# Performance work log

Measured on AMD Instinct MI355X. Metric: run time of the kernel, lower is better.

Reference implementation:

```python
import jax, jax.numpy as jnp
import numpy as np

N_EMBED = 1024
N_HEAD = 16
EPS = 1.1920929e-07  # torch.finfo(float32).eps, nn.RMSNorm default eps=None


def rmsnorm(x, w):
    var = jnp.mean(x * x, axis=-1, keepdims=True)
    return x * jax.lax.rsqrt(var + EPS) * w


def setup_inputs() -> dict:
    key = jax.random.key(0)
    ks = jax.random.split(key, 12)
    d = N_EMBED
    s = lambda fan_in: 1.0 / np.sqrt(fan_in)
    inp = {
        "x": jax.random.normal(ks[0], (2, 2048, d), jnp.float32),
        "w_attn": jax.random.uniform(ks[1], (d, 3 * d), jnp.float32, -s(d), s(d)),
        "b_attn": jax.random.uniform(ks[2], (3 * d,), jnp.float32, -s(d), s(d)),
        "w_proj": jax.random.uniform(ks[3], (d, d), jnp.float32, -s(d), s(d)),
        "b_proj": jax.random.uniform(ks[4], (d,), jnp.float32, -s(d), s(d)),
        "w_fc1": jax.random.uniform(ks[5], (d, 4 * d), jnp.float32, -s(d), s(d)),
        "b_fc1": jax.random.uniform(ks[6], (4 * d,), jnp.float32, -s(d), s(d)),
        "w_fc2": jax.random.uniform(ks[7], (4 * d, d), jnp.float32, -s(4 * d), s(4 * d)),
        "b_fc2": jax.random.uniform(ks[8], (d,), jnp.float32, -s(4 * d), s(4 * d)),
        "g_norm1": jnp.ones((d,), jnp.float32),
        "g_norm2": jnp.ones((d,), jnp.float32),
    }
    return inp


def reference(x, w_attn, b_attn, w_proj, b_proj, w_fc1, b_fc1, w_fc2, b_fc2, g_norm1, g_norm2):
    B, T, d = x.shape
    H = N_HEAD
    hd = d // H

    # --- attention branch ---
    h = rmsnorm(x, g_norm1)
    qkv = h @ w_attn + b_attn  # [B,T,3d]
    q, k, v = jnp.split(qkv, 3, axis=-1)
    q = q.reshape(B, T, H, hd).transpose(0, 2, 1, 3)  # [B,H,T,hd]
    k = k.reshape(B, T, H, hd).transpose(0, 2, 1, 3)
    v = v.reshape(B, T, H, hd).transpose(0, 2, 1, 3)
    qk = jnp.einsum('bhqd,bhkd->bhqk', q, k)  # NOTE: no logit scaling (as in source)
    mask = jnp.tril(jnp.ones((T, T), bool))
    qk = jnp.where(mask, qk, -jnp.inf)
    # source scales softmax OUTPUT by n_embed**-0.5 (faithful quirk)
    attn = jax.nn.softmax(qk, axis=-1) * (d ** -0.5)
    o = jnp.einsum('bhqk,bhkd->bhqd', attn, v)
    o = o.transpose(0, 2, 1, 3).reshape(B, T, d)
    x = x + (o @ w_proj + b_proj)

    # --- MLP branch ---
    h = rmsnorm(x, g_norm2)
    h = jax.nn.gelu(h @ w_fc1 + b_fc1, approximate=False)
    x = x + (h @ w_fc2 + b_fc2)
    return x
```

## Files before the change

kernel.cpp:

```cpp
#include <hip/hip_runtime.h>
#include <hip/hip_bf16.h>


typedef __hip_bfloat16 bf16;
typedef __attribute__((ext_vector_type(8))) short short8;
typedef __attribute__((ext_vector_type(4))) float floatx4;

__device__ __forceinline__ float bits2f(unsigned short u) {
  union { unsigned int i; float f; } c; c.i = ((unsigned int)u) << 16; return c.f;
}
__device__ __forceinline__ unsigned short f2bits(float f) {
  bf16 b = __float2bfloat16(f);
  union { bf16 b; unsigned short u; } c; c.b = b; return c.u;
}

__device__ __forceinline__ void gld_lds16(const unsigned short* g, unsigned short* l) {
  __builtin_amdgcn_global_load_lds(
      (const __attribute__((address_space(1))) void*)g,
      (__attribute__((address_space(3))) void*)l, 16, 0, 0);
}

__global__ __launch_bounds__(256) void rmsnorm_r9(const float* __restrict__ x,
                                                  const float* __restrict__ g,
                                                  unsigned short* __restrict__ out)
{
  const int row = blockIdx.x, tid = threadIdx.x;
  const size_t rb = (size_t)row * 1024;
  float4 xv = *(const float4*)(x + rb + tid * 4);
  float v[4] = {xv.x, xv.y, xv.z, xv.w};
  float s = v[0]*v[0] + v[1]*v[1] + v[2]*v[2] + v[3]*v[3];
  #pragma unroll
  for (int off = 32; off > 0; off >>= 1) s += __shfl_down(s, off, 64);
  __shared__ float part[4];
  if ((tid & 63) == 0) part[tid >> 6] = s;
  __syncthreads();
  const float tot = part[0] + part[1] + part[2] + part[3];
  const float sc = rsqrtf(tot * (1.0f / 1024.0f) + 1.1920929e-07f);
  float4 gv = *(const float4*)(g + tid * 4);
  ushort4 o4 = { f2bits(v[0] * sc * gv.x), f2bits(v[1] * sc * gv.y),
                 f2bits(v[2] * sc * gv.z), f2bits(v[3] * sc * gv.w) };
  *(ushort4*)(out + rb + tid * 4) = o4;
}

__global__ __launch_bounds__(256) void wprep_r9(const float* __restrict__ in,
                                                unsigned short* __restrict__ out,
                                                int K, int N)
{
  __shared__ unsigned short tile[32][33];
  const int tid = threadIdx.x;
  const int k0 = blockIdx.y * 32, n0 = blockIdx.x * 32;
  const int tr = tid >> 3, tc4 = (tid & 7) * 4;
  float4 v = *(const float4*)(in + (size_t)(k0 + tr) * N + n0 + tc4);
  tile[tr][tc4 + 0] = f2bits(v.x);
  tile[tr][tc4 + 1] = f2bits(v.y);
  tile[tr][tc4 + 2] = f2bits(v.z);
  tile[tr][tc4 + 3] = f2bits(v.w);
  __syncthreads();
  ushort4 o = { tile[tc4 + 0][tr], tile[tc4 + 1][tr],
                tile[tc4 + 2][tr], tile[tc4 + 3][tr] };
  *(ushort4*)(out + (size_t)(n0 + tr) * K + k0 + tc4) = o;
}

template<int EPI>
__global__ __launch_bounds__(256) void gemm_r9(
    const unsigned short* __restrict__ A,
    const unsigned short* __restrict__ BT,
    const float* __restrict__ bias,
    const float* __restrict__ resid,
    void* __restrict__ Cout,
    int M, int N, int K)
{
  __shared__ __align__(16) unsigned short As[128 * 32];
  __shared__ __align__(16) unsigned short Bs[128 * 32];
  const int tid = threadIdx.x;
  const int lane = tid & 63;
  const int wv = tid >> 6;
  const int m0 = blockIdx.y * 128, n0 = blockIdx.x * 128;
  const int wm = (wv >> 1) * 64, wn = (wv & 1) * 64;

  const int s0 = tid, s1 = tid + 256;
  const int r0 = s0 >> 2, kq0 = (s0 & 3) ^ ((r0 >> 1) & 3);
  const int r1 = s1 >> 2, kq1 = (s1 & 3) ^ ((r1 >> 1) & 3);
  const unsigned short* Ab = A  + (size_t)m0 * K;
  const unsigned short* Bb = BT + (size_t)n0 * K;
  const size_t ga0 = (size_t)r0 * K + kq0 * 8;
  const size_t ga1 = (size_t)r1 * K + kq1 * 8;

  floatx4 acc[4][4];
  #pragma unroll
  for (int i = 0; i < 4; ++i)
    #pragma unroll
    for (int j = 0; j < 4; ++j)
      acc[i][j] = (floatx4){0.f, 0.f, 0.f, 0.f};

  int aoff[4], boff[4];
  #pragma unroll
  for (int i = 0; i < 4; ++i) {
    int ra = wm + i * 16 + (lane & 15);
    aoff[i] = (ra * 4 + ((lane >> 4) ^ ((ra >> 1) & 3))) * 8;
    int rb = wn + i * 16 + (lane & 15);
    boff[i] = (rb * 4 + ((lane >> 4) ^ ((rb >> 1) & 3))) * 8;
  }

  for (int k0 = 0; k0 < K; k0 += 32) {
    __syncthreads();
    gld_lds16(Ab + ga0 + k0, As + s0 * 8);
    gld_lds16(Ab + ga1 + k0, As + s1 * 8);
    gld_lds16(Bb + ga0 + k0, Bs + s0 * 8);
    gld_lds16(Bb + ga1 + k0, Bs + s1 * 8);
    __syncthreads();

    short8 af[4], bfr[4];
    #pragma unroll
    for (int i = 0; i < 4; ++i) {
      af[i]  = *(const short8*)(As + aoff[i]);
      bfr[i] = *(const short8*)(Bs + boff[i]);
    }
    #pragma unroll
    for (int i = 0; i < 4; ++i)
      #pragma unroll
      for (int j = 0; j < 4; ++j)
        acc[i][j] = __builtin_amdgcn_mfma_f32_16x16x32_bf16(af[i], bfr[j], acc[i][j], 0, 0, 0);
  }

  #pragma unroll
  for (int i = 0; i < 4; ++i) {
    #pragma unroll
    for (int j = 0; j < 4; ++j) {
      const int rbase = m0 + wm + i * 16 + (lane >> 4) * 4;
      const int c = n0 + wn + j * 16 + (lane & 15);
      const float bia = bias[c];
      #pragma unroll
      for (int r = 0; r < 4; ++r) {
        float v = acc[i][j][r] + bia;
        const size_t idx = (size_t)(rbase + r) * N + c;
        if constexpr (EPI == 0) {
          ((unsigned short*)Cout)[idx] = f2bits(v);
        } else if constexpr (EPI == 1) {
          ((float*)Cout)[idx] = v + resid[idx];
        } else if constexpr (EPI == 2) {
          v = 0.5f * v * (1.0f + erff(v * 0.70710678118654752f));
          ((unsigned short*)Cout)[idx] = f2bits(v);
        } else {
          ((float*)Cout)[idx] = v + resid[idx];
        }
      }
    }
  }
}

__global__ __launch_bounds__(512) void attn_r9(const unsigned short* __restrict__ qkv,
                                               unsigned short* __restrict__ o)
{
  __shared__ __align__(16) unsigned short Qs[128 * 64];
  __shared__ __align__(16) unsigned short Ks[2][64 * 64];
  __shared__ __align__(16) unsigned short VT[2][64 * 72];
  __shared__ __align__(16) unsigned short Ps[128 * 72];
  __shared__ __align__(16) float stat_s[128];

  const int tid = threadIdx.x, lane = tid & 63, wv = tid >> 6;
  const int quad = lane >> 4, l15 = lane & 15;
  const int qt0 = blockIdx.x, bh = blockIdx.y;
  const int b = bh >> 4, h = bh & 15;
  const size_t base = (size_t)b * 2048 * 3072;
  const int qcol = h * 64, kcol = 1024 + h * 64, vcol = 2048 + h * 64;

  const int sr = tid >> 3, scp = tid & 7, sc = scp ^ (sr & 7);
  const unsigned short* kgp = qkv + base + (size_t)sr * 3072 + kcol + sc * 8;
  const int vp = tid & 31, vdc = tid >> 5;
  const unsigned short* vgp = qkv + base + (size_t)(2 * vp) * 3072 + vcol + vdc * 4;

  for (int pass = 0; pass < 2; ++pass) {
    const int qt = pass ? qt0 : 15 - qt0;
    const int q0 = qt * 128;
    const int nkt = 2 * qt + 2;

    __syncthreads();

    #pragma unroll
    for (int p = 0; p < 2; ++p) {
      int s = tid + 512 * p;
      int r = s >> 3, cp = s & 7, c = cp ^ (r & 7);
      gld_lds16(qkv + base + (size_t)(q0 + r) * 3072 + qcol + c * 8, Qs + s * 8);
    }
    gld_lds16(kgp, Ks[0] + tid * 8);
    {
      uint2 u0 = *(const uint2*)vgp;
      uint2 u1 = *(const uint2*)(vgp + 3072);
      unsigned short* dst = VT[0] + (size_t)(vdc * 4) * 72 + 2 * vp;
      *(unsigned int*)(dst + 0 * 72) = (u0.x & 0xffffu) | (u1.x << 16);
      *(unsigned int*)(dst + 1 * 72) = (u0.x >> 16)     | (u1.x & 0xffff0000u);
      *(unsigned int*)(dst + 2 * 72) = (u0.y & 0xffffu) | (u1.y << 16);
      *(unsigned int*)(dst + 3 * 72) = (u0.y >> 16)     | (u1.y & 0xffff0000u);
    }
    __syncthreads();

    short8 qa[2];
    #pragma unroll
    for (int ks = 0; ks < 2; ++ks) {
      int ra = wv * 16 + l15;
      int cp = (ks * 4 + quad) ^ (ra & 7);
      qa[ks] = *(const short8*)(Qs + (ra * 8 + cp) * 8);
    }

    floatx4 oacc[4];
    #pragma unroll
    for (int dt = 0; dt < 4; ++dt) oacc[dt] = (floatx4){0.f, 0.f, 0.f, 0.f};
    float m_i[4], l_i[4];
    #pragma unroll
    for (int r = 0; r < 4; ++r) { m_i[r] = -3.0e38f; l_i[r] = 0.0f; }

    for (int kt = 0; kt < nkt; ++kt) {
      const int cur = kt & 1;
      const bool pf = (kt + 1 < nkt);
      uint2 u0, u1;
      if (pf) {
        const size_t koff = (size_t)(kt + 1) * 64 * 3072;
        gld_lds16(kgp + koff, Ks[cur ^ 1] + tid * 8);
        u0 = *(const uint2*)(vgp + koff);
        u1 = *(const uint2*)(vgp + koff + 3072);
      }

      short8 kb[4][2];
      #pragma unroll
      for (int j = 0; j < 4; ++j)
        #pragma unroll
        for (int ks = 0; ks < 2; ++ks) {
          int rb = j * 16 + l15;
          int cp = (ks * 4 + quad) ^ (rb & 7);
          kb[j][ks] = *(const short8*)(Ks[cur] + (rb * 8 + cp) * 8);
        }
      floatx4 s_[4];
      #pragma unroll
      for (int j = 0; j < 4; ++j) s_[j] = (floatx4){0.f, 0.f, 0.f, 0.f};
      #pragma unroll
      for (int j = 0; j < 4; ++j)
        #pragma unroll
        for (int ks = 0; ks < 2; ++ks)
          s_[j] = __builtin_amdgcn_mfma_f32_16x16x32_bf16(qa[ks], kb[j][ks], s_[j], 0, 0, 0);

      const int k0 = kt * 64;
      const int rowmin = q0 + wv * 16;
      const int rowb = rowmin + quad * 4;
      if (k0 + 63 > rowmin) {
        #pragma unroll
        for (int j = 0; j < 4; ++j) {
          const int col = k0 + j * 16 + l15;
          #pragma unroll
          for (int r = 0; r < 4; ++r)
            if (col > rowb + r) s_[j][r] = -3.0e38f;
        }
      }
      float fm[4], al[4], rs[4];
      #pragma unroll
      for (int r = 0; r < 4; ++r)
        fm[r] = fmaxf(fmaxf(s_[0][r], s_[1][r]), fmaxf(s_[2][r], s_[3][r]));
      #pragma unroll
      for (int msk = 1; msk < 16; msk <<= 1)
        #pragma unroll
        for (int r = 0; r < 4; ++r)
          fm[r] = fmaxf(fm[r], __shfl_xor(fm[r], msk, 64));
      #pragma unroll
      for (int r = 0; r < 4; ++r) {
        const float mn = fmaxf(m_i[r], fm[r]);
        al[r] = __expf(m_i[r] - mn);
        m_i[r] = mn;
      }
      #pragma unroll
      for (int j = 0; j < 4; ++j)
        #pragma unroll
        for (int r = 0; r < 4; ++r)
          s_[j][r] = __expf(s_[j][r] - m_i[r]);
      #pragma unroll
      for (int r = 0; r < 4; ++r)
        rs[r] = (s_[0][r] + s_[1][r]) + (s_[2][r] + s_[3][r]);
      #pragma unroll
      for (int msk = 1; msk < 16; msk <<= 1)
        #pragma unroll
        for (int r = 0; r < 4; ++r)
          rs[r] += __shfl_xor(rs[r], msk, 64);
      #pragma unroll
      for (int r = 0; r < 4; ++r)
        l_i[r] = l_i[r] * al[r] + rs[r];
      if (l15 == 0) {
        float4 a4 = { al[0], al[1], al[2], al[3] };
        *(float4*)(stat_s + wv * 16 + quad * 4) = a4;
      }
      #pragma unroll
      for (int j = 0; j < 4; ++j)
        #pragma unroll
        for (int r = 0; r < 4; ++r)
          Ps[(size_t)(wv * 16 + quad * 4 + r) * 72 + j * 16 + l15] = f2bits(s_[j][r]);

      const float alq = stat_s[wv * 16 + l15];
      #pragma unroll
      for (int dt = 0; dt < 4; ++dt)
        #pragma unroll
        for (int r = 0; r < 4; ++r)
          oacc[dt][r] *= alq;

      short8 va[4][2], pb[2];
      #pragma unroll
      for (int dt = 0; dt < 4; ++dt)
        #pragma unroll
        for (int ks = 0; ks < 2; ++ks)
          va[dt][ks] = *(const short8*)(VT[cur] + (size_t)(dt * 16 + l15) * 72 + ks * 32 + quad * 8);
      #pragma unroll
      for (int ks = 0; ks < 2; ++ks)
        pb[ks] = *(const short8*)(Ps + (size_t)(wv * 16 + l15) * 72 + ks * 32 + quad * 8);
      #pragma unroll
      for (int dt = 0; dt < 4; ++dt)
        #pragma unroll
        for (int ks = 0; ks < 2; ++ks)
          oacc[dt] = __builtin_amdgcn_mfma_f32_16x16x32_bf16(va[dt][ks], pb[ks], oacc[dt], 0, 0, 0);

      if (pf) {
        unsigned short* dst = VT[cur ^ 1] + (size_t)(vdc * 4) * 72 + 2 * vp;
        *(unsigned int*)(dst + 0 * 72) = (u0.x & 0xffffu) | (u1.x << 16);
        *(unsigned int*)(dst + 1 * 72) = (u0.x >> 16)     | (u1.x & 0xffff0000u);
        *(unsigned int*)(dst + 2 * 72) = (u0.y & 0xffffu) | (u1.y << 16);
        *(unsigned int*)(dst + 3 * 72) = (u0.y >> 16)     | (u1.y & 0xffff0000u);
      }
      __syncthreads();
    }

    if (l15 == 0) {
      float4 l4 = { l_i[0], l_i[1], l_i[2], l_i[3] };
      *(float4*)(stat_s + wv * 16 + quad * 4) = l4;
    }
    const float linv = 0.03125f / stat_s[wv * 16 + l15];
    const size_t row = (size_t)b * 2048 + q0 + wv * 16 + l15;
    #pragma unroll
    for (int dt = 0; dt < 4; ++dt) {
      const int col = h * 64 + dt * 16 + quad * 4;
      ushort4 o4 = { f2bits(oacc[dt][0] * linv), f2bits(oacc[dt][1] * linv),
                     f2bits(oacc[dt][2] * linv), f2bits(oacc[dt][3] * linv) };
      *(ushort4*)(o + row * 1024 + col) = o4;
    }
  }
}

extern "C" void kernel_launch(void* const* d_in, const int* in_sizes, int n_in,
                              void* d_out, int out_size, void* d_ws, size_t ws_size,
                              hipStream_t stream)
{
  (void)in_sizes; (void)n_in; (void)out_size; (void)ws_size;
  const float* x      = (const float*)d_in[0];
  const float* w_attn = (const float*)d_in[1];
  const float* b_attn = (const float*)d_in[2];
  const float* w_proj = (const float*)d_in[3];
  const float* b_proj = (const float*)d_in[4];
  const float* w_fc1  = (const float*)d_in[5];
  const float* b_fc1  = (const float*)d_in[6];
  const float* w_fc2  = (const float*)d_in[7];
  const float* b_fc2  = (const float*)d_in[8];
  const float* g1     = (const float*)d_in[9];
  const float* g2     = (const float*)d_in[10];
  float* out = (float*)d_out;

  char* ws = (char*)d_ws;
  unsigned short* h   = (unsigned short*)(ws);
  unsigned short* qkv = (unsigned short*)(ws + ((size_t)8  << 20));
  unsigned short* ov  = (unsigned short*)(ws);
  float*          x1  = (float*)         (ws + ((size_t)32 << 20));
  unsigned short* h2  = (unsigned short*)(ws + ((size_t)8  << 20));
  unsigned short* h3  = (unsigned short*)(ws + ((size_t)48 << 20));
  unsigned short* WT  = (unsigned short*)(ws + ((size_t)80 << 20));

  const int M = 4096;

  rmsnorm_r9<<<M, 256, 0, stream>>>(x, g1, h);
  wprep_r9<<<dim3(3072 / 32, 1024 / 32), 256, 0, stream>>>(w_attn, WT, 1024, 3072);
  gemm_r9<0><<<dim3(3072 / 128, M / 128), 256, 0, stream>>>(h, WT, b_attn, nullptr, qkv, M, 3072, 1024);
  attn_r9<<<dim3(8, 32), 512, 0, stream>>>(qkv, ov);
  wprep_r9<<<dim3(1024 / 32, 1024 / 32), 256, 0, stream>>>(w_proj, WT, 1024, 1024);
  gemm_r9<1><<<dim3(1024 / 128, M / 128), 256, 0, stream>>>(ov, WT, b_proj, x, x1, M, 1024, 1024);
  rmsnorm_r9<<<M, 256, 0, stream>>>(x1, g2, h2);
  wprep_r9<<<dim3(4096 / 32, 1024 / 32), 256, 0, stream>>>(w_fc1, WT, 1024, 4096);
  gemm_r9<2><<<dim3(4096 / 128, M / 128), 256, 0, stream>>>(h2, WT, b_fc1, nullptr, h3, M, 4096, 1024);
  wprep_r9<<<dim3(1024 / 32, 4096 / 32), 256, 0, stream>>>(w_fc2, WT, 4096, 1024);
  gemm_r9<3><<<dim3(1024 / 128, M / 128), 256, 0, stream>>>(h3, WT, b_fc2, x1, out, M, 1024, 4096);
}
```

Measured before the change: 418.6 us.

## Double-buffer GEMM LDS loads and split-K the FC2 GEMM

The GEMM main loop now uses two LDS buffers and issues the global-to-LDS loads for the next K step before the MFMAs on the current one, with one barrier per iteration instead of two. The FC2 GEMM, which has only 256 output tiles, is split along K into two halves that write fp32 partials. A new reduction kernel then sums the partials with the bias and residual. This trades extra LDS, partial-sum memory traffic and one more launch for overlap of loads with compute and more parallelism on the long-K GEMM.

```diff
diff --git a/kernel.cpp b/kernel.cpp
--- a/kernel.cpp
+++ b/kernel.cpp
@@ -20,9 +20,9 @@
       (__attribute__((address_space(3))) void*)l, 16, 0, 0);
 }
 
-__global__ __launch_bounds__(256) void rmsnorm_r9(const float* __restrict__ x,
-                                                  const float* __restrict__ g,
-                                                  unsigned short* __restrict__ out)
+__global__ __launch_bounds__(256) void rmsnorm_r10(const float* __restrict__ x,
+                                                   const float* __restrict__ g,
+                                                   unsigned short* __restrict__ out)
 {
   const int row = blockIdx.x, tid = threadIdx.x;
   const size_t rb = (size_t)row * 1024;
@@ -42,9 +42,9 @@
   *(ushort4*)(out + rb + tid * 4) = o4;
 }
 
-__global__ __launch_bounds__(256) void wprep_r9(const float* __restrict__ in,
-                                                unsigned short* __restrict__ out,
-                                                int K, int N)
+__global__ __launch_bounds__(256) void wprep_r10(const float* __restrict__ in,
+                                                 unsigned short* __restrict__ out,
+                                                 int K, int N)
 {
   __shared__ unsigned short tile[32][33];
   const int tid = threadIdx.x;
@@ -62,29 +62,30 @@
 }
 
 template<int EPI>
-__global__ __launch_bounds__(256) void gemm_r9(
+__global__ __launch_bounds__(256) void gemm_r10(
     const unsigned short* __restrict__ A,
     const unsigned short* __restrict__ BT,
     const float* __restrict__ bias,
     const float* __restrict__ resid,
     void* __restrict__ Cout,
-    int M, int N, int K)
-{
-  __shared__ __align__(16) unsigned short As[128 * 32];
-  __shared__ __align__(16) unsigned short Bs[128 * 32];
+    int M, int N, int K, int Klen)
+{
+  __shared__ __align__(16) unsigned short As[2][128 * 32];
+  __shared__ __align__(16) unsigned short Bs[2][128 * 32];
   const int tid = threadIdx.x;
   const int lane = tid & 63;
   const int wv = tid >> 6;
   const int m0 = blockIdx.y * 128, n0 = blockIdx.x * 128;
   const int wm = (wv >> 1) * 64, wn = (wv & 1) * 64;
+  const int kbase = blockIdx.z * Klen;
 
   const int s0 = tid, s1 = tid + 256;
   const int r0 = s0 >> 2, kq0 = (s0 & 3) ^ ((r0 >> 1) & 3);
   const int r1 = s1 >> 2, kq1 = (s1 & 3) ^ ((r1 >> 1) & 3);
   const unsigned short* Ab = A  + (size_t)m0 * K;
   const unsigned short* Bb = BT + (size_t)n0 * K;
-  const size_t ga0 = (size_t)r0 * K + kq0 * 8;
-  const size_t ga1 = (size_t)r1 * K + kq1 * 8;
+  const size_t ga0 = (size_t)r0 * K + kq0 * 8 + kbase;
+  const size_t ga1 = (size_t)r1 * K + kq1 * 8 + kbase;
 
   floatx4 acc[4][4];
   #pragma unroll
@@ -102,26 +103,40 @@
     boff[i] = (rb * 4 + ((lane >> 4) ^ ((rb >> 1) & 3))) * 8;
   }
 
-  for (int k0 = 0; k0 < K; k0 += 32) {
-    __syncthreads();
-    gld_lds16(Ab + ga0 + k0, As + s0 * 8);
-    gld_lds16(Ab + ga1 + k0, As + s1 * 8);
-    gld_lds16(Bb + ga0 + k0, Bs + s0 * 8);
-    gld_lds16(Bb + ga1 + k0, Bs + s1 * 8);
-    __syncthreads();
+  gld_lds16(Ab + ga0, As[0] + s0 * 8);
+  gld_lds16(Ab + ga1, As[0] + s1 * 8);
+  gld_lds16(Bb + ga0, Bs[0] + s0 * 8);
+  gld_lds16(Bb + ga1, Bs[0] + s1 * 8);
+  __syncthreads();
+
+  const int nsteps = Klen >> 5;
+  for (int t = 0; t < nsteps; ++t) {
+    const int cur = t & 1;
+    if (t + 1 < nsteps) {
+      const size_t ko = (size_t)(t + 1) * 32;
+      gld_lds16(Ab + ga0 + ko, As[cur ^ 1] + s0 * 8);
+      gld_lds16(Ab + ga1 + ko, As[cur ^ 1] + s1 * 8);
+      gld_lds16(Bb + ga0 + ko, Bs[cur ^ 1] + s0 * 8);
+      gld_lds16(Bb + ga1 + ko, Bs[cur ^ 1] + s1 * 8);
+    }
 
     short8 af[4], bfr[4];
     #pragma unroll
     for (int i = 0; i < 4; ++i) {
-      af[i]  = *(const short8*)(As + aoff[i]);
-      bfr[i] = *(const short8*)(Bs + boff[i]);
+      af[i]  = *(const short8*)(As[cur] + aoff[i]);
+      bfr[i] = *(const short8*)(Bs[cur] + boff[i]);
     }
     #pragma unroll
     for (int i = 0; i < 4; ++i)
       #pragma unroll
       for (int j = 0; j < 4; ++j)
         acc[i][j] = __builtin_amdgcn_mfma_f32_16x16x32_bf16(af[i], bfr[j], acc[i][j], 0, 0, 0);
+
+    __syncthreads();
   }
+
+  float* Cp32 = (float*)Cout;
+  if constexpr (EPI == 4) Cp32 += (size_t)blockIdx.z * ((size_t)M * N);
 
   #pragma unroll
   for (int i = 0; i < 4; ++i) {
@@ -129,7 +144,8 @@
     for (int j = 0; j < 4; ++j) {
       const int rbase = m0 + wm + i * 16 + (lane >> 4) * 4;
       const int c = n0 + wn + j * 16 + (lane & 15);
-      const float bia = bias[c];
+      float bia = 0.0f;
+      if constexpr (EPI != 4) bia = bias[c];
       #pragma unroll
       for (int r = 0; r < 4; ++r) {
         float v = acc[i][j][r] + bia;
@@ -141,16 +157,34 @@
         } else if constexpr (EPI == 2) {
           v = 0.5f * v * (1.0f + erff(v * 0.70710678118654752f));
           ((unsigned short*)Cout)[idx] = f2bits(v);
+        } else if constexpr (EPI == 3) {
+          ((float*)Cout)[idx] = v + resid[idx];
         } else {
-          ((float*)Cout)[idx] = v + resid[idx];
+          Cp32[idx] = v;
         }
       }
     }
   }
 }
 
-__global__ __launch_bounds__(512) void attn_r9(const unsigned short* __restrict__ qkv,
-                                               unsigned short* __restrict__ o)
+__global__ __launch_bounds__(256) void red2_r10(const float* __restrict__ P,
+                                                const float* __restrict__ resid,
+                                                const float* __restrict__ bias,
+                                                float* __restrict__ out)
+{
+  const size_t i = ((size_t)blockIdx.x * 256 + threadIdx.x) * 4;
+  const int col = (int)(i & 1023);
+  float4 p0 = *(const float4*)(P + i);
+  float4 p1 = *(const float4*)(P + ((size_t)4096 * 1024) + i);
+  float4 xr = *(const float4*)(resid + i);
+  float4 b  = *(const float4*)(bias + col);
+  float4 o  = { p0.x + p1.x + xr.x + b.x, p0.y + p1.y + xr.y + b.y,
+                p0.z + p1.z + xr.z + b.z, p0.w + p1.w + xr.w + b.w };
+  *(float4*)(out + i) = o;
+}
+
+__global__ __launch_bounds__(512) void attn_r10(const unsigned short* __restrict__ qkv,
+                                                unsigned short* __restrict__ o)
 {
   __shared__ __align__(16) unsigned short Qs[128 * 64];
   __shared__ __align__(16) unsigned short Ks[2][64 * 64];
@@ -366,18 +400,20 @@
   unsigned short* h2  = (unsigned short*)(ws + ((size_t)8  << 20));
   unsigned short* h3  = (unsigned short*)(ws + ((size_t)48 << 20));
   unsigned short* WT  = (unsigned short*)(ws + ((size_t)80 << 20));
+  float*          P   = (float*)(ws);
 
   const int M = 4096;
 
-  rmsnorm_r9<<<M, 256, 0, stream>>>(x, g1, h);
-  wprep_r9<<<dim3(3072 / 32, 1024 / 32), 256, 0, stream>>>(w_attn, WT, 1024, 3072);
-  gemm_r9<0><<<dim3(3072 / 128, M / 128), 256, 0, stream>>>(h, WT, b_attn, nullptr, qkv, M, 3072, 1024);
-  attn_r9<<<dim3(8, 32), 512, 0, stream>>>(qkv, ov);
-  wprep_r9<<<dim3(1024 / 32, 1024 / 32), 256, 0, stream>>>(w_proj, WT, 1024, 1024);
-  gemm_r9<1><<<dim3(1024 / 128, M / 128), 256, 0, stream>>>(ov, WT, b_proj, x, x1, M, 1024, 1024);
-  rmsnorm_r9<<<M, 256, 0, stream>>>(x1, g2, h2);
-  wprep_r9<<<dim3(4096 / 32, 1024 / 32), 256, 0, stream>>>(w_fc1, WT, 1024, 4096);
-  gemm_r9<2><<<dim3(4096 / 128, M / 128), 256, 0, stream>>>(h2, WT, b_fc1, nullptr, h3, M, 4096, 1024);
-  wprep_r9<<<dim3(1024 / 32, 4096 / 32), 256, 0, stream>>>(w_fc2, WT, 4096, 1024);
-  gemm_r9<3><<<dim3(1024 / 128, M / 128), 256, 0, stream>>>(h3, WT, b_fc2, x1, out, M, 1024, 4096);
-}
+  rmsnorm_r10<<<M, 256, 0, stream>>>(x, g1, h);
+  wprep_r10<<<dim3(3072 / 32, 1024 / 32), 256, 0, stream>>>(w_attn, WT, 1024, 3072);
+  gemm_r10<0><<<dim3(3072 / 128, M / 128), 256, 0, stream>>>(h, WT, b_attn, nullptr, qkv, M, 3072, 1024, 1024);
+  attn_r10<<<dim3(8, 32), 512, 0, stream>>>(qkv, ov);
+  wprep_r10<<<dim3(1024 / 32, 1024 / 32), 256, 0, stream>>>(w_proj, WT, 1024, 1024);
+  gemm_r10<1><<<dim3(1024 / 128, M / 128), 256, 0, stream>>>(ov, WT, b_proj, x, x1, M, 1024, 1024, 1024);
+  rmsnorm_r10<<<M, 256, 0, stream>>>(x1, g2, h2);
+  wprep_r10<<<dim3(4096 / 32, 1024 / 32), 256, 0, stream>>>(w_fc1, WT, 1024, 4096);
+  gemm_r10<2><<<dim3(4096 / 128, M / 128), 256, 0, stream>>>(h2, WT, b_fc1, nullptr, h3, M, 4096, 1024, 1024);
+  wprep_r10<<<dim3(1024 / 32, 4096 / 32), 256, 0, stream>>>(w_fc2, WT, 4096, 1024);
+  gemm_r10<4><<<dim3(1024 / 128, M / 128, 2), 256, 0, stream>>>(h3, WT, nullptr, nullptr, P, M, 1024, 4096, 2048);
+  red2_r10<<<4096, 256, 0, stream>>>(P, x1, b_fc2, out);
+}
```

Result: faster. 386.5 us (-7.7%).
